# Kernel optimization log

Measured on AMD Instinct MI355X. Metric: run time of the kernel, lower is better.

## Reference

```python
import jax, jax.numpy as jnp
import numpy as np

N_HEAD = 50000
N_TAIL = 50000
E = 800000
F_IN = 256
D = 64
H = 4
FE = 64
N_ETYPES = 5
NEG_SLOPE = 0.2


def setup_inputs() -> dict:
    key = jax.random.key(0)
    ks = jax.random.split(key, 10)
    head_feature = jax.random.normal(ks[0], (N_HEAD, F_IN), jnp.float32)
    tail_feature = jax.random.normal(ks[1], (N_TAIL, F_IN), jnp.float32)
    head_ind = jax.random.randint(ks[2], (E,), 0, N_HEAD)
    tail_ind = jax.random.randint(ks[3], (E,), 0, N_TAIL)
    edge_list = jnp.stack([head_ind, tail_ind], axis=0)  # [2, E]
    tmp_edge = jax.random.randint(ks[4], (E,), 0, N_ETYPES)
    s = 0.05  # small init scale, mimics uniform(-stdv, stdv)
    W = jax.random.normal(ks[5], (F_IN, D * H), jnp.float32) * s
    W_e = jax.random.normal(ks[6], (FE, FE * H), jnp.float32) * s
    edge_emb = jax.random.normal(ks[7], (N_ETYPES, FE), jnp.float32) * s
    a_l = jax.random.normal(ks[8], (1, H, D), jnp.float32) * s
    a_r = jax.random.normal(jax.random.fold_in(ks[8], 1), (1, H, D), jnp.float32) * s
    a_e = jax.random.normal(ks[9], (1, H, FE), jnp.float32) * s
    return {
        "head_feature": head_feature,
        "tail_feature": tail_feature,
        "edge_list": edge_list,
        "tmp_edge": tmp_edge,
        "W": W,
        "W_e": W_e,
        "edge_emb": edge_emb,
        "a_l": a_l,
        "a_r": a_r,
        "a_e": a_e,
    }


def _layer(head_feature, tail_feature, head_ind, tail_ind, tmp_edge,
           W, W_e, edge_emb, a_l, a_r, a_e):
    n_head = head_feature.shape[0]
    # dense projections (dropout = identity in eval)
    h_head = (head_feature @ W).reshape(-1, H, D)      # [N_h, H, D]
    h_tail = (tail_feature @ W).reshape(-1, H, D)      # [N_t, H, D]
    e = (edge_emb @ W_e).reshape(-1, H, FE)            # [T, H, FE]
    # per-edge attention logits
    h_l = (a_l * h_head).sum(-1)[head_ind]             # [E, H]
    h_r = (a_r * h_tail).sum(-1)[tail_ind]             # [E, H]
    h_e = (a_e * e).sum(-1)[tmp_edge]                  # [E, H]
    score = jax.nn.leaky_relu(h_l + h_r + h_e, NEG_SLOPE)
    # segment softmax over edges grouped by destination (head) node, per head
    m = jax.ops.segment_max(score, head_ind, num_segments=n_head)   # [N_h, H]
    ex = jnp.exp(score - m[head_ind])                               # [E, H]
    z = jax.ops.segment_sum(ex, head_ind, num_segments=n_head)      # [N_h, H]
    alpha = ex / z[head_ind]                                        # [E, H]
    # weighted aggregation: sparse-mm per head, vectorized over heads
    msg = alpha[:, :, None] * h_tail[tail_ind]                      # [E, H, D]
    out = jax.ops.segment_sum(msg, head_ind, num_segments=n_head)   # [N_h, H, D]
    out = out.reshape(n_head, H * D)
    return jax.nn.elu(out)


def reference(head_feature, tail_feature, edge_list, tmp_edge,
              W, W_e, edge_emb, a_l, a_r, a_e):
    head_ind = edge_list[0]
    tail_ind = edge_list[1]
    return _layer(head_feature, tail_feature, head_ind, tail_ind, tmp_edge,
                  W, W_e, edge_emb, a_l, a_r, a_e)
```

## Files before the change

kernel.cpp:

```cpp
#include <hip/hip_runtime.h>
#include <hip/hip_bf16.h>
#include <math.h>

#define N_HEADN 50000
#define N_TAILN 50000
#define NE      800000
#define F_IN    256
#define HH      4
#define HD      256
#define FE      64
#define N_ETYPES 5
#define NEG_SLOPE 0.2f
#define NB_SCAN ((N_HEADN + 255) / 256)
#define NB_CVT  ((N_TAILN * F_IN) / (256 * 16))
#define NB_HIST (NE / 256)
#define NB_PROJ ((N_TAILN + 63) / 64)

typedef __attribute__((ext_vector_type(8))) short bf16x8;
typedef __attribute__((ext_vector_type(4))) float f32x4;

static __device__ __forceinline__ unsigned short f2bf(float f) {
    unsigned u = __float_as_uint(f);
    return (unsigned short)((u + 0x7FFF + ((u >> 16) & 1)) >> 16);
}
static __device__ __forceinline__ float bf2f(unsigned short u) {
    return __uint_as_float((unsigned)u << 16);
}

__global__ __launch_bounds__(256) void prep_kernel(const int* __restrict__ head,
                                                   int* __restrict__ counts,
                                                   const float* __restrict__ X,
                                                   unsigned short* __restrict__ Xb,
                                                   const float* __restrict__ W,
                                                   const float* __restrict__ a_l,
                                                   const float* __restrict__ W_e,
                                                   const float* __restrict__ a_e,
                                                   const float* __restrict__ edge_emb,
                                                   float* __restrict__ waT,
                                                   float* __restrict__ heo,
                                                   short* __restrict__ Wt) {
    const int b = blockIdx.x;
    if (b < NB_HIST) {
        int e = b * 256 + threadIdx.x;
        atomicAdd(&counts[head[e]], 1);
    } else if (b < NB_HIST + NB_CVT) {
        size_t t = (size_t)(b - NB_HIST) * 256 + threadIdx.x;
        const float4* xp = (const float4*)X + t * 4;
        float4 v0 = xp[0], v1 = xp[1], v2 = xp[2], v3 = xp[3];
        bf16x8 o0, o1;
        o0[0] = (short)f2bf(v0.x); o0[1] = (short)f2bf(v0.y);
        o0[2] = (short)f2bf(v0.z); o0[3] = (short)f2bf(v0.w);
        o0[4] = (short)f2bf(v1.x); o0[5] = (short)f2bf(v1.y);
        o0[6] = (short)f2bf(v1.z); o0[7] = (short)f2bf(v1.w);
        o1[0] = (short)f2bf(v2.x); o1[1] = (short)f2bf(v2.y);
        o1[2] = (short)f2bf(v2.z); o1[3] = (short)f2bf(v2.w);
        o1[4] = (short)f2bf(v3.x); o1[5] = (short)f2bf(v3.y);
        o1[6] = (short)f2bf(v3.z); o1[7] = (short)f2bf(v3.w);
        bf16x8* op = (bf16x8*)(Xb + t * 16);
        op[0] = o0;
        op[1] = o1;
    } else if (b == NB_HIST + NB_CVT) {
        int k = threadIdx.x;
        #pragma unroll
        for (int h = 0; h < HH; ++h) {
            float s = 0.f;
            for (int d = 0; d < 64; ++d) s += a_l[h * 64 + d] * W[(size_t)k * HD + h * 64 + d];
            waT[h * 256 + k] = s;
        }
    } else if (b == NB_HIST + NB_CVT + 1) {
        __shared__ float wae[FE][HH];
        int t = threadIdx.x;
        int k = t >> 2, h = t & 3;
        float s = 0.f;
        for (int f = 0; f < 64; ++f) s += a_e[h * 64 + f] * W_e[(size_t)k * (FE * HH) + h * 64 + f];
        wae[k][h] = s;
        __syncthreads();
        if (t < N_ETYPES * HH) {
            int ty = t >> 2, hh = t & 3;
            float acc = 0.f;
            for (int kk = 0; kk < FE; ++kk) acc += edge_emb[ty * FE + kk] * wae[kk][hh];
            heo[ty * HH + hh] = acc;
        }
    } else {
        int n = b - (NB_HIST + NB_CVT + 2), k = threadIdx.x;
        Wt[(size_t)n * 256 + k] = (short)f2bf(W[(size_t)k * 256 + n]);
    }
}

__global__ void blocksum_kernel(const int* __restrict__ counts, int* __restrict__ blockSums) {
    __shared__ int s[256];
    int t = threadIdx.x, j = blockIdx.x * 256 + t;
    s[t] = (j < N_HEADN) ? counts[j] : 0;
    __syncthreads();
    for (int off = 128; off > 0; off >>= 1) {
        if (t < off) s[t] += s[t + off];
        __syncthreads();
    }
    if (t == 0) blockSums[blockIdx.x] = s[0];
}

__global__ void blockscan_kernel(const int* __restrict__ blockSums, int* __restrict__ blockOff) {
    __shared__ int s[256];
    int t = threadIdx.x;
    int v = (t < NB_SCAN) ? blockSums[t] : 0;
    s[t] = v;
    __syncthreads();
    for (int off = 1; off < 256; off <<= 1) {
        int u = (t >= off) ? s[t - off] : 0;
        __syncthreads();
        s[t] += u;
        __syncthreads();
    }
    if (t < NB_SCAN) blockOff[t] = s[t] - v;
}

__global__ void rowstart_kernel(const int* __restrict__ counts, const int* __restrict__ blockOff,
                                int* __restrict__ row_start, int* __restrict__ cursor) {
    __shared__ int s[256];
    int t = threadIdx.x, j = blockIdx.x * 256 + t;
    int c = (j < N_HEADN) ? counts[j] : 0;
    s[t] = c;
    __syncthreads();
    for (int off = 1; off < 256; off <<= 1) {
        int u = (t >= off) ? s[t - off] : 0;
        __syncthreads();
        s[t] += u;
        __syncthreads();
    }
    int excl = blockOff[blockIdx.x] + s[t] - c;
    if (j < N_HEADN) {
        row_start[j] = excl;
        cursor[j]    = excl;
        if (j == N_HEADN - 1) row_start[N_HEADN] = excl + c;
    }
}

__global__ __launch_bounds__(256) void hd_proj_kernel(const float* __restrict__ Xh,
                                                      const float* __restrict__ waT,
                                                      float* __restrict__ hl,
                                                      const unsigned short* __restrict__ Xb,
                                                      const short* __restrict__ Wt,
                                                      const float* __restrict__ a,
                                                      unsigned short* __restrict__ h_out,
                                                      float* __restrict__ dot_out,
                                                      int N) {
    if (blockIdx.x < NB_PROJ) {
        const int tid  = threadIdx.x;
        const int w    = tid >> 6;
        const int lane = tid & 63;
        const int quad = lane >> 4;
        const int l15  = lane & 15;
        const int n0   = blockIdx.x * 64;

        int rbase[4];
        #pragma unroll
        for (int mt = 0; mt < 4; ++mt) {
            int r = n0 + mt * 16;
            rbase[mt] = (r + 16 <= N) ? r : (N - 16);
        }

        f32x4 acc[4][4];
        #pragma unroll
        for (int mt = 0; mt < 4; ++mt)
            #pragma unroll
            for (int ct = 0; ct < 4; ++ct)
                acc[mt][ct] = (f32x4){0.f, 0.f, 0.f, 0.f};

        const short* wbase = Wt + (size_t)(w * 64 + l15) * 256 + quad * 8;
        const unsigned short* xb[4];
        #pragma unroll
        for (int mt = 0; mt < 4; ++mt)
            xb[mt] = Xb + (size_t)(rbase[mt] + l15) * F_IN + quad * 8;

        #pragma unroll 2
        for (int k0 = 0; k0 < 256; k0 += 32) {
            bf16x8 af[4];
            #pragma unroll
            for (int mt = 0; mt < 4; ++mt) af[mt] = *(const bf16x8*)(xb[mt] + k0);
            #pragma unroll
            for (int ct = 0; ct < 4; ++ct) {
                bf16x8 bfrag = *(const bf16x8*)(wbase + (size_t)ct * 16 * 256 + k0);
                #pragma unroll
                for (int mt = 0; mt < 4; ++mt)
                    acc[mt][ct] = __builtin_amdgcn_mfma_f32_16x16x32_bf16(af[mt], bfrag, acc[mt][ct], 0, 0, 0);
            }
        }

        float av[4];
        #pragma unroll
        for (int ct = 0; ct < 4; ++ct) av[ct] = a[w * 64 + ct * 16 + l15];

        #pragma unroll
        for (int mt = 0; mt < 4; ++mt) {
            #pragma unroll
            for (int ct = 0; ct < 4; ++ct) {
                #pragma unroll
                for (int r = 0; r < 4; ++r) {
                    int row = rbase[mt] + quad * 4 + r;
                    h_out[(size_t)row * HD + w * 64 + ct * 16 + l15] = f2bf(acc[mt][ct][r]);
                }
            }
            #pragma unroll
            for (int r = 0; r < 4; ++r) {
                float p = av[0] * acc[mt][0][r] + av[1] * acc[mt][1][r]
                        + av[2] * acc[mt][2][r] + av[3] * acc[mt][3][r];
                p += __shfl_xor(p, 1);
                p += __shfl_xor(p, 2);
                p += __shfl_xor(p, 4);
                p += __shfl_xor(p, 8);
                if (l15 == 0) {
                    int row = rbase[mt] + quad * 4 + r;
                    dot_out[(size_t)row * HH + w] = p;
                }
            }
        }
    } else {
        const int wave = threadIdx.x >> 6;
        const int lane = threadIdx.x & 63;
        const int n = (blockIdx.x - NB_PROJ) * 4 + wave;
        float4 x = ((const float4*)(Xh + (size_t)n * F_IN))[lane];
        float p[HH];
        #pragma unroll
        for (int h = 0; h < HH; ++h) {
            float4 w = ((const float4*)(waT + h * 256))[lane];
            p[h] = x.x * w.x + x.y * w.y + x.z * w.z + x.w * w.w;
        }
        #pragma unroll
        for (int off = 1; off < 64; off <<= 1) {
            #pragma unroll
            for (int h = 0; h < HH; ++h) p[h] += __shfl_xor(p[h], off);
        }
        if (lane < HH) hl[(size_t)n * HH + lane] = p[lane];
    }
}

__global__ void scatter_kernel(const int* __restrict__ head, const int* __restrict__ tail,
                               const int* __restrict__ etype,
                               const float* __restrict__ hl, const float* __restrict__ hr,
                               const float* __restrict__ he,
                               int* __restrict__ cursor, int* __restrict__ packed,
                               float* __restrict__ exE) {
    int e = blockIdx.x * 256 + threadIdx.x;
    int h0 = head[e];
    int tl = tail[e];
    int ty = etype[e];
    float4 L = *(const float4*)(hl + (size_t)h0 * HH);
    float4 R = *(const float4*)(hr + (size_t)tl * HH);
    float4 T = *(const float4*)(he + ty * HH);
    float s0 = L.x + R.x + T.x;
    float s1 = L.y + R.y + T.y;
    float s2 = L.z + R.z + T.z;
    float s3 = L.w + R.w + T.w;
    s0 = (s0 > 0.f) ? s0 : NEG_SLOPE * s0;
    s1 = (s1 > 0.f) ? s1 : NEG_SLOPE * s1;
    s2 = (s2 > 0.f) ? s2 : NEG_SLOPE * s2;
    s3 = (s3 > 0.f) ? s3 : NEG_SLOPE * s3;
    float w0 = __expf(s0), w1 = __expf(s1), w2 = __expf(s2), w3 = __expf(s3);
    int pos = atomicAdd(&cursor[h0], 1);
    packed[pos] = tl;
    *(float4*)(exE + (size_t)pos * HH) = make_float4(w0, w1, w2, w3);
}

__global__ __launch_bounds__(256) void agg_kernel(const int* __restrict__ row_start,
                                                  const int* __restrict__ packed,
                                                  const float* __restrict__ exE,
                                                  const unsigned short* __restrict__ h_tail,
                                                  float* __restrict__ out) {
    const int wave = threadIdx.x >> 6;
    const int lane = threadIdx.x & 63;
    const int n = blockIdx.x * 4 + wave;
    const int s = row_start[n];
    const int e = row_start[n + 1];
    const int g = lane >> 5;
    const int q = lane & 31;
    const int h = q >> 3;

    float acc[8];
    #pragma unroll
    for (int c = 0; c < 8; ++c) acc[c] = 0.f;
    float z = 0.f;

    for (int base = s; base < e; base += 64) {
        const int cnt = (e - base < 64) ? (e - base) : 64;
        int myidx = 0;
        if (base + lane < e) myidx = packed[base + lane];
        #pragma unroll 8
        for (int i = 0; i < cnt; i += 2) {
            const int j = i + g;
            const int tl = __shfl(myidx, j);
            if (j < cnt) {
                const float w = exE[(size_t)(base + j) * HH + h];
                uint4 u = *(const uint4*)(h_tail + (size_t)tl * HD + q * 8);
                #pragma unroll
                for (int d = 0; d < 4; ++d) {
                    unsigned uu = ((const unsigned*)&u)[d];
                    acc[2 * d]     += w * __uint_as_float(uu << 16);
                    acc[2 * d + 1] += w * __uint_as_float(uu & 0xFFFF0000u);
                }
                z += w;
            }
        }
    }

    #pragma unroll
    for (int c = 0; c < 8; ++c) acc[c] += __shfl_xor(acc[c], 32);
    z += __shfl_xor(z, 32);

    float4 o;
    if (z > 0.f) {
        o.x = acc[4 * g + 0] / z;
        o.y = acc[4 * g + 1] / z;
        o.z = acc[4 * g + 2] / z;
        o.w = acc[4 * g + 3] / z;
        o.x = (o.x > 0.f) ? o.x : expm1f(o.x);
        o.y = (o.y > 0.f) ? o.y : expm1f(o.y);
        o.z = (o.z > 0.f) ? o.z : expm1f(o.z);
        o.w = (o.w > 0.f) ? o.w : expm1f(o.w);
    } else {
        o = make_float4(0.f, 0.f, 0.f, 0.f);
    }
    ((float4*)(out + (size_t)n * HD))[q * 2 + g] = o;
}

extern "C" void kernel_launch(void* const* d_in, const int* in_sizes, int n_in,
                              void* d_out, int out_size, void* d_ws, size_t ws_size,
                              hipStream_t stream) {
    const float* head_feature = (const float*)d_in[0];
    const float* tail_feature = (const float*)d_in[1];
    const int*   edge_list    = (const int*)d_in[2];
    const int*   tmp_edge     = (const int*)d_in[3];
    const float* W            = (const float*)d_in[4];
    const float* W_e          = (const float*)d_in[5];
    const float* edge_emb     = (const float*)d_in[6];
    const float* a_l          = (const float*)d_in[7];
    const float* a_r          = (const float*)d_in[8];
    const float* a_e          = (const float*)d_in[9];
    const int* head_ind = edge_list;
    const int* tail_ind = edge_list + NE;

    char* ws = (char*)d_ws;
    unsigned short* h_tail = (unsigned short*)ws; ws += sizeof(unsigned short) * (size_t)N_TAILN * HD;
    unsigned short* Xb = (unsigned short*)ws;
    float* exE    = (float*)(void*)Xb;
    int*   packed = (int*)(void*)((char*)(void*)Xb + sizeof(float) * (size_t)NE * HH);
    ws += sizeof(unsigned short) * (size_t)N_TAILN * HD;
    short* Wt        = (short*)ws; ws += sizeof(short) * 256 * 256;
    float* hl        = (float*)ws; ws += sizeof(float) * (size_t)N_HEADN * HH;
    float* hr        = (float*)ws; ws += sizeof(float) * (size_t)N_TAILN * HH;
    float* waT       = (float*)ws; ws += sizeof(float) * HH * 256;
    float* he        = (float*)ws; ws += sizeof(float) * 32;
    int*   counts    = (int*)ws;   ws += sizeof(int) * (size_t)N_HEADN;
    int*   row_start = (int*)ws;   ws += sizeof(int) * (size_t)(N_HEADN + 4);
    int*   cursor    = (int*)ws;   ws += sizeof(int) * (size_t)N_HEADN;
    int*   blockSums = (int*)ws;   ws += sizeof(int) * 256;
    int*   blockOff  = (int*)ws;   ws += sizeof(int) * 256;

    hipMemsetAsync(counts, 0, sizeof(int) * (size_t)N_HEADN, stream);

    hipLaunchKernelGGL(prep_kernel, dim3(NB_HIST + NB_CVT + 258), dim3(256), 0, stream,
                       head_ind, counts, tail_feature, Xb,
                       W, a_l, W_e, a_e, edge_emb, waT, he, Wt);

    hipLaunchKernelGGL(blocksum_kernel, dim3(NB_SCAN), dim3(256), 0, stream,
                       counts, blockSums);
    hipLaunchKernelGGL(blockscan_kernel, dim3(1), dim3(256), 0, stream,
                       blockSums, blockOff);
    hipLaunchKernelGGL(rowstart_kernel, dim3(NB_SCAN), dim3(256), 0, stream,
                       counts, blockOff, row_start, cursor);

    hipLaunchKernelGGL(hd_proj_kernel, dim3(NB_PROJ + N_HEADN / 4), dim3(256), 0, stream,
                       head_feature, waT, hl,
                       Xb, Wt, a_r, h_tail, hr, N_TAILN);

    hipLaunchKernelGGL(scatter_kernel, dim3(NE / 256), dim3(256), 0, stream,
                       head_ind, tail_ind, tmp_edge, hl, hr, he, cursor, packed, exE);

    hipLaunchKernelGGL(agg_kernel, dim3(N_HEADN / 4), dim3(256), 0, stream,
                       row_start, packed, exE, h_tail, (float*)d_out);
}
```

Before: 364.8 us.

## Split fused projection kernel and parallelize tail GEMM across heads with register-held weights

Splits the combined head-dot/tail-projection kernel into two separate launches. The MFMA tail projection now gives each block one head and 64 rows, so there are 4x more blocks. Each wave keeps its 16-column weight slice in registers for the whole K loop, and the per-head attention dot is reduced across waves through shared memory. The aim is more parallelism and lower register pressure per wave. The cost is an extra kernel launch, and each X tile is re-read by 4 blocks.

New measurement: 383.8 us. 1.05x slower.

```diff
diff --git a/kernel.cpp b/kernel.cpp
--- a/kernel.cpp
+++ b/kernel.cpp
@@ -135,102 +135,100 @@
     }
 }
 
-__global__ __launch_bounds__(256) void hd_proj_kernel(const float* __restrict__ Xh,
-                                                      const float* __restrict__ waT,
-                                                      float* __restrict__ hl,
-                                                      const unsigned short* __restrict__ Xb,
-                                                      const short* __restrict__ Wt,
-                                                      const float* __restrict__ a,
-                                                      unsigned short* __restrict__ h_out,
-                                                      float* __restrict__ dot_out,
-                                                      int N) {
-    if (blockIdx.x < NB_PROJ) {
-        const int tid  = threadIdx.x;
-        const int w    = tid >> 6;
-        const int lane = tid & 63;
-        const int quad = lane >> 4;
-        const int l15  = lane & 15;
-        const int n0   = blockIdx.x * 64;
-
-        int rbase[4];
-        #pragma unroll
-        for (int mt = 0; mt < 4; ++mt) {
-            int r = n0 + mt * 16;
-            rbase[mt] = (r + 16 <= N) ? r : (N - 16);
-        }
-
-        f32x4 acc[4][4];
+__global__ __launch_bounds__(256) void head_dot_kernel(const float* __restrict__ X,
+                                                       const float* __restrict__ waT,
+                                                       float* __restrict__ hl) {
+    const int wave = threadIdx.x >> 6;
+    const int lane = threadIdx.x & 63;
+    const int n = blockIdx.x * 4 + wave;
+    float4 x = ((const float4*)(X + (size_t)n * F_IN))[lane];
+    float p[HH];
+    #pragma unroll
+    for (int h = 0; h < HH; ++h) {
+        float4 w = ((const float4*)(waT + h * 256))[lane];
+        p[h] = x.x * w.x + x.y * w.y + x.z * w.z + x.w * w.w;
+    }
+    #pragma unroll
+    for (int off = 1; off < 64; off <<= 1) {
+        #pragma unroll
+        for (int h = 0; h < HH; ++h) p[h] += __shfl_xor(p[h], off);
+    }
+    if (lane < HH) hl[(size_t)n * HH + lane] = p[lane];
+}
+
+__global__ __launch_bounds__(256) void proj_mfma_kernel(const unsigned short* __restrict__ Xb,
+                                                        const short* __restrict__ Wt,
+                                                        const float* __restrict__ a,
+                                                        unsigned short* __restrict__ h_out,
+                                                        float* __restrict__ hr,
+                                                        int N) {
+    const int head = blockIdx.x & 3;
+    const int n0   = (blockIdx.x >> 2) * 64;
+    const int wv   = threadIdx.x >> 6;
+    const int lane = threadIdx.x & 63;
+    const int quad = lane >> 4;
+    const int l15  = lane & 15;
+
+    __shared__ float hrbuf[4][64];
+
+    int rbase[4];
+    #pragma unroll
+    for (int mt = 0; mt < 4; ++mt) {
+        int r = n0 + mt * 16;
+        rbase[mt] = (r + 16 <= N) ? r : (N - 16);
+    }
+
+    const short* wbase = Wt + (size_t)(head * 64 + wv * 16 + l15) * 256 + quad * 8;
+    bf16x8 breg[8];
+    #pragma unroll
+    for (int kk = 0; kk < 8; ++kk) breg[kk] = *(const bf16x8*)(wbase + kk * 32);
+
+    f32x4 acc[4];
+    #pragma unroll
+    for (int mt = 0; mt < 4; ++mt) acc[mt] = (f32x4){0.f, 0.f, 0.f, 0.f};
+
+    const unsigned short* xrow[4];
+    #pragma unroll
+    for (int mt = 0; mt < 4; ++mt)
+        xrow[mt] = Xb + (size_t)(rbase[mt] + l15) * F_IN + quad * 8;
+
+    #pragma unroll
+    for (int kk = 0; kk < 8; ++kk) {
+        bf16x8 af[4];
+        #pragma unroll
+        for (int mt = 0; mt < 4; ++mt) af[mt] = *(const bf16x8*)(xrow[mt] + kk * 32);
         #pragma unroll
         for (int mt = 0; mt < 4; ++mt)
-            #pragma unroll
-            for (int ct = 0; ct < 4; ++ct)
-                acc[mt][ct] = (f32x4){0.f, 0.f, 0.f, 0.f};
-
-        const short* wbase = Wt + (size_t)(w * 64 + l15) * 256 + quad * 8;
-        const unsigned short* xb[4];
-        #pragma unroll
-        for (int mt = 0; mt < 4; ++mt)
-            xb[mt] = Xb + (size_t)(rbase[mt] + l15) * F_IN + quad * 8;
-
-        #pragma unroll 2
-        for (int k0 = 0; k0 < 256; k0 += 32) {
-            bf16x8 af[4];
-            #pragma unroll
-            for (int mt = 0; mt < 4; ++mt) af[mt] = *(const bf16x8*)(xb[mt] + k0);
-            #pragma unroll
-            for (int ct = 0; ct < 4; ++ct) {
-                bf16x8 bfrag = *(const bf16x8*)(wbase + (size_t)ct * 16 * 256 + k0);
-                #pragma unroll
-                for (int mt = 0; mt < 4; ++mt)
-                    acc[mt][ct] = __builtin_amdgcn_mfma_f32_16x16x32_bf16(af[mt], bfrag, acc[mt][ct], 0, 0, 0);
-            }
-        }
-
-        float av[4];
-        #pragma unroll
-        for (int ct = 0; ct < 4; ++ct) av[ct] = a[w * 64 + ct * 16 + l15];
-
-        #pragma unroll
-        for (int mt = 0; mt < 4; ++mt) {
-            #pragma unroll
-            for (int ct = 0; ct < 4; ++ct) {
-                #pragma unroll
-                for (int r = 0; r < 4; ++r) {
-                    int row = rbase[mt] + quad * 4 + r;
-                    h_out[(size_t)row * HD + w * 64 + ct * 16 + l15] = f2bf(acc[mt][ct][r]);
-                }
-            }
-            #pragma unroll
-            for (int r = 0; r < 4; ++r) {
-                float p = av[0] * acc[mt][0][r] + av[1] * acc[mt][1][r]
-                        + av[2] * acc[mt][2][r] + av[3] * acc[mt][3][r];
-                p += __shfl_xor(p, 1);
-                p += __shfl_xor(p, 2);
-                p += __shfl_xor(p, 4);
-                p += __shfl_xor(p, 8);
-                if (l15 == 0) {
-                    int row = rbase[mt] + quad * 4 + r;
-                    dot_out[(size_t)row * HH + w] = p;
-                }
-            }
-        }
-    } else {
-        const int wave = threadIdx.x >> 6;
-        const int lane = threadIdx.x & 63;
-        const int n = (blockIdx.x - NB_PROJ) * 4 + wave;
-        float4 x = ((const float4*)(Xh + (size_t)n * F_IN))[lane];
-        float p[HH];
-        #pragma unroll
-        for (int h = 0; h < HH; ++h) {
-            float4 w = ((const float4*)(waT + h * 256))[lane];
-            p[h] = x.x * w.x + x.y * w.y + x.z * w.z + x.w * w.w;
-        }
-        #pragma unroll
-        for (int off = 1; off < 64; off <<= 1) {
-            #pragma unroll
-            for (int h = 0; h < HH; ++h) p[h] += __shfl_xor(p[h], off);
-        }
-        if (lane < HH) hl[(size_t)n * HH + lane] = p[lane];
+            acc[mt] = __builtin_amdgcn_mfma_f32_16x16x32_bf16(af[mt], breg[kk], acc[mt], 0, 0, 0);
+    }
+
+    const float av = a[head * 64 + wv * 16 + l15];
+
+    #pragma unroll
+    for (int mt = 0; mt < 4; ++mt) {
+        #pragma unroll
+        for (int r = 0; r < 4; ++r) {
+            int row = rbase[mt] + quad * 4 + r;
+            h_out[(size_t)row * HD + head * 64 + wv * 16 + l15] = f2bf(acc[mt][r]);
+        }
+        #pragma unroll
+        for (int r = 0; r < 4; ++r) {
+            float p = av * acc[mt][r];
+            p += __shfl_xor(p, 1);
+            p += __shfl_xor(p, 2);
+            p += __shfl_xor(p, 4);
+            p += __shfl_xor(p, 8);
+            if (l15 == 0) hrbuf[wv][mt * 16 + quad * 4 + r] = p;
+        }
+    }
+    __syncthreads();
+    if (threadIdx.x < 64) {
+        int row = threadIdx.x;
+        int mt  = row >> 4;
+        int rb  = (n0 + mt * 16 + 16 <= N) ? (n0 + mt * 16) : (N - 16);
+        int g   = rb + (row & 15);
+        float s = hrbuf[0][row] + hrbuf[1][row] + hrbuf[2][row] + hrbuf[3][row];
+        hr[(size_t)g * HH + head] = s;
     }
 }
 
@@ -368,8 +366,9 @@
     hipLaunchKernelGGL(rowstart_kernel, dim3(NB_SCAN), dim3(256), 0, stream,
                        counts, blockOff, row_start, cursor);
 
-    hipLaunchKernelGGL(hd_proj_kernel, dim3(NB_PROJ + N_HEADN / 4), dim3(256), 0, stream,
-                       head_feature, waT, hl,
+    hipLaunchKernelGGL(head_dot_kernel, dim3(N_HEADN / 4), dim3(256), 0, stream,
+                       head_feature, waT, hl);
+    hipLaunchKernelGGL(proj_mfma_kernel, dim3(NB_PROJ * 4), dim3(256), 0, stream,
                        Xb, Wt, a_r, h_tail, hr, N_TAILN);
 
     hipLaunchKernelGGL(scatter_kernel, dim3(NE / 256), dim3(256), 0, stream,
```
